# Performance work log

Measured on AMD Instinct MI355X. Metric: run time of the kernel, lower is better.

The kernel has to match this reference:

```python
import jax, jax.numpy as jnp
import numpy as np

# Module hyperparameters (from __init__ defaults / init_kwargs)
A_PLUS = 0.005
A_MINUS = 0.00525
TAU_PLUS = 20.0
TAU_MINUS = 20.0
DT = 1.0

B, T, N_PRE, N_POST = 512, 100, 256, 256
SPIKE_RATE = 0.1


def setup_inputs() -> dict:
    key = jax.random.key(0)
    k1, k2, k3 = jax.random.split(key, 3)
    pre_spikes = (jax.random.uniform(k1, (B, T, N_PRE)) < SPIKE_RATE).astype(jnp.float32)
    post_spikes = (jax.random.uniform(k2, (B, T, N_POST)) < SPIKE_RATE).astype(jnp.float32)
    weights = jax.random.uniform(k3, (N_PRE, N_POST), dtype=jnp.float32)
    return {"pre_spikes": pre_spikes, "post_spikes": post_spikes, "weights": weights}


def _pre_trace(pre_tbn, decay):
    """trace[t] = sum_{tau=1..t} decay^tau * pre[t-tau]  (exact recurrence).

    pre_tbn: [T, B, N]. Returns [T, B, N] with trace[0] = 0.
    """
    def step(carry, x_t):
        # emit trace[t] = carry, then carry' = decay * (carry + pre[t])
        return decay * (carry + x_t), carry
    _, trace = jax.lax.scan(step, jnp.zeros_like(pre_tbn[0]), pre_tbn)
    return trace


def reference(pre_spikes, post_spikes, weights):
    """Classical STDP weight update.

    With T <= int(tau_plus*5) the original nested t/tau loops equal:
      dW[p,q] = (1/(B*T)) * sum_{t,b} (A+ * trace+[t,b,p] - A- * trace-[t,b,p]) * post[b,t,q]
    where trace+/- are exponential pre-synaptic eligibility traces.
    """
    batch, time_steps, _ = pre_spikes.shape
    pre_t = jnp.transpose(pre_spikes, (1, 0, 2))    # [T, B, n_pre]
    post_t = jnp.transpose(post_spikes, (1, 0, 2))  # [T, B, n_post]

    decay_plus = jnp.exp(jnp.float32(-DT / TAU_PLUS))
    decay_minus = jnp.exp(jnp.float32(-DT / TAU_MINUS))

    trace_plus = _pre_trace(pre_t, decay_plus)    # LTP: pre fires before post
    trace_minus = _pre_trace(pre_t, decay_minus)  # LTD: pre fires before post (depression of reversed pairing)

    eff = A_PLUS * trace_plus - A_MINUS * trace_minus  # [T, B, n_pre]
    weight_update = jnp.einsum('tbp,tbq->pq', eff, post_t) / (batch * time_steps)
    # original initializes update as zeros_like(weights); output shape matches weights
    return weight_update + jnp.zeros_like(weights)
```

## Files before the change

kernel.cpp:

```cpp
#include <hip/hip_runtime.h>
#include <stdint.h>

#define B_SZ   512
#define T_SZ   100
#define NPRE   256
#define NPOST  256
#define KTOT   (B_SZ * T_SZ)

typedef __bf16 bf16x8 __attribute__((ext_vector_type(8)));
typedef float  floatx4 __attribute__((ext_vector_type(4)));

__device__ __forceinline__ uint32_t bf16_rne(float v) {
    uint32_t bits = __float_as_uint(v);
    return (bits + 0x7FFFu + ((bits >> 16) & 1u)) >> 16;
}
__device__ __forceinline__ uint32_t pack_trunc2(float a, float b) {
    return (__float_as_uint(a) >> 16) | (__float_as_uint(b) & 0xFFFF0000u);
}

__global__ __launch_bounds__(256, 2) void stdp_fused_gemm(
    const float* __restrict__ pre, const float* __restrict__ post,
    float* __restrict__ partial)
{
    __shared__ __align__(16) unsigned short A_lds[32][512];
    __shared__ __align__(16) unsigned short B_lds[32][512];

    const int bx   = blockIdx.x;
    const int s    = bx & 127;
    const int tile = bx >> 7;
    const int pt   = tile & 1;
    const int qt   = tile >> 1;
    const int tid  = threadIdx.x;
    const int lane = tid & 63, wave = tid >> 6;
    const int l15 = lane & 15, l4 = lane >> 4;

    const int half  = tid >> 7;
    const int p_loc = tid & 127;
    const int qloc  = tid & 127;
    const int qg = qloc >> 4, q15 = qloc & 15;

    const float decay = 0.95122942450071400910f;

    floatx4 acc[2][8] = {};

    for (int r = 0; r < 2; ++r) {
        uint32_t pk[50];
        {
            const int b = s * 4 + 2 * r + half;
            const float* src = pre + (size_t)b * (T_SZ * NPRE) + pt * 128 + p_loc;
            float carry = 0.0f;
#pragma unroll
            for (int kc = 0; kc < 3; ++kc) {
                float x[32];
#pragma unroll
                for (int j = 0; j < 32; ++j)
                    x[j] = src[(size_t)(kc * 32 + j) * NPRE];
#pragma unroll
                for (int j = 0; j < 16; ++j) {
                    uint32_t lo = bf16_rne(carry);
                    carry = decay * (carry + x[2 * j]);
                    uint32_t hi = bf16_rne(carry);
                    carry = decay * (carry + x[2 * j + 1]);
                    pk[kc * 16 + j] = lo | (hi << 16);
                }
            }
            float x[4];
#pragma unroll
            for (int j = 0; j < 4; ++j)
                x[j] = src[(size_t)(96 + j) * NPRE];
#pragma unroll
            for (int j = 0; j < 2; ++j) {
                uint32_t lo = bf16_rne(carry);
                carry = decay * (carry + x[2 * j]);
                uint32_t hi = bf16_rne(carry);
                carry = decay * (carry + x[2 * j + 1]);
                pk[48 + j] = lo | (hi << 16);
            }
        }

        for (int lh = 0; lh < 2; ++lh) {
            const int b = s * 4 + 2 * r + lh;

            if (half == lh) {
                const int pg = p_loc >> 4, lp = p_loc & 15;
#pragma unroll
                for (int kc = 0; kc < 3; ++kc)
#pragma unroll
                    for (int w = 0; w < 4; ++w)
                        *(uint4*)&A_lds[kc * 8 + pg][(w * 16 + lp) * 8] =
                            make_uint4(pk[kc * 16 + w * 4],     pk[kc * 16 + w * 4 + 1],
                                       pk[kc * 16 + w * 4 + 2], pk[kc * 16 + w * 4 + 3]);
                *(uint4*)&A_lds[24 + pg][lp * 8] = make_uint4(pk[48], pk[49], 0u, 0u);
#pragma unroll
                for (int w = 1; w < 4; ++w)
                    *(uint4*)&A_lds[24 + pg][(w * 16 + lp) * 8] =
                        make_uint4(0u, 0u, 0u, 0u);
            }

            const float* pb = post + (size_t)b * (T_SZ * NPOST) + qt * 128 + qloc;
            if (half == 0) {
                float x[48];
#pragma unroll
                for (int j = 0; j < 48; ++j)
                    x[j] = pb[(size_t)j * NPOST];
#pragma unroll
                for (int o = 0; o < 6; ++o)
                    *(uint4*)&B_lds[(o >> 2) * 8 + qg][((o & 3) * 16 + q15) * 8] =
                        make_uint4(pack_trunc2(x[o * 8 + 0], x[o * 8 + 1]),
                                   pack_trunc2(x[o * 8 + 2], x[o * 8 + 3]),
                                   pack_trunc2(x[o * 8 + 4], x[o * 8 + 5]),
                                   pack_trunc2(x[o * 8 + 6], x[o * 8 + 7]));
            } else {
                float x[52];
#pragma unroll
                for (int j = 0; j < 52; ++j)
                    x[j] = pb[(size_t)(48 + j) * NPOST];
#pragma unroll
                for (int o = 6; o < 12; ++o) {
                    int u = o * 8 - 48;
                    *(uint4*)&B_lds[(o >> 2) * 8 + qg][((o & 3) * 16 + q15) * 8] =
                        make_uint4(pack_trunc2(x[u + 0], x[u + 1]),
                                   pack_trunc2(x[u + 2], x[u + 3]),
                                   pack_trunc2(x[u + 4], x[u + 5]),
                                   pack_trunc2(x[u + 6], x[u + 7]));
                }
                *(uint4*)&B_lds[24 + qg][q15 * 8] =
                    make_uint4(pack_trunc2(x[48], x[49]), pack_trunc2(x[50], x[51]), 0u, 0u);
#pragma unroll
                for (int o = 13; o < 16; ++o)
                    *(uint4*)&B_lds[24 + qg][((o & 3) * 16 + q15) * 8] =
                        make_uint4(0u, 0u, 0u, 0u);
            }
            __syncthreads();

#pragma unroll
            for (int kc = 0; kc < 4; ++kc) {
                bf16x8 a[2], bb[8];
#pragma unroll
                for (int f = 0; f < 2; ++f)
                    a[f] = *(const bf16x8*)&A_lds[kc * 8 + wave * 2 + f][lane * 8];
#pragma unroll
                for (int g = 0; g < 8; ++g)
                    bb[g] = *(const bf16x8*)&B_lds[kc * 8 + g][lane * 8];
#pragma unroll
                for (int f = 0; f < 2; ++f)
#pragma unroll
                    for (int g = 0; g < 8; ++g)
                        acc[f][g] = __builtin_amdgcn_mfma_f32_16x16x32_bf16(
                            a[f], bb[g], acc[f][g], 0, 0, 0);
            }
            __syncthreads();
        }
    }

    float* pout = partial + (size_t)bx * (128 * 128);
#pragma unroll
    for (int f = 0; f < 2; ++f) {
        int r0 = wave * 32 + f * 16 + l4 * 4;
#pragma unroll
        for (int g = 0; g < 8; ++g) {
            int c = g * 16 + l15;
#pragma unroll
            for (int v = 0; v < 4; ++v)
                pout[(size_t)(r0 + v) * 128 + c] = acc[f][g][v];
        }
    }
}

__global__ __launch_bounds__(256) void stdp_reduce1(
    const float* __restrict__ partial, float* __restrict__ tmp)
{
    const int t = blockIdx.x * 256 + threadIdx.x;
    const int g = t >> 16;
    const int e = t & 65535;
    const int tile = e >> 14;
    const float* src = partial + ((size_t)(tile * 128 + g * 16) << 14) + (e & 16383);
    float a4[4] = {};
#pragma unroll
    for (int i = 0; i < 4; ++i)
#pragma unroll
        for (int u = 0; u < 4; ++u)
            a4[u] += src[(size_t)(u * 4 + i) << 14];
    tmp[t] = (a4[0] + a4[1]) + (a4[2] + a4[3]);
}

__global__ __launch_bounds__(256) void stdp_reduce2(
    const float* __restrict__ tmp, float* __restrict__ out)
{
    const int idx = blockIdx.x * 256 + threadIdx.x;
    const int P = idx >> 8, Q = idx & 255;
    const int tile = (Q >> 7) * 2 + (P >> 7);
    const int e = (tile << 14) | ((P & 127) << 7) | (Q & 127);
    float a[4];
#pragma unroll
    for (int u = 0; u < 4; ++u)
        a[u] = tmp[(size_t)(2 * u) * 65536 + e] +
               tmp[(size_t)(2 * u + 1) * 65536 + e];
    const float scale = (0.005f - 0.00525f) * (1.0f / (float)KTOT);
    out[idx] = ((a[0] + a[1]) + (a[2] + a[3])) * scale;
}

extern "C" void kernel_launch(void* const* d_in, const int* in_sizes, int n_in,
                              void* d_out, int out_size, void* d_ws, size_t ws_size,
                              hipStream_t stream)
{
    const float* pre  = (const float*)d_in[0];
    const float* post = (const float*)d_in[1];
    float* out = (float*)d_out;

    float* partial = (float*)d_ws;
    float* tmp     = (float*)((char*)d_ws + (size_t)33554432);

    stdp_fused_gemm<<<512, 256, 0, stream>>>(pre, post, partial);
    stdp_reduce1<<<2048, 256, 0, stream>>>(partial, tmp);
    stdp_reduce2<<<256, 256, 0, stream>>>(tmp, out);
}
```

Measured before the change: 140.4 us.

## Double block size to 512 threads, computing all four batch traces in one pass

The GEMM kernel now runs 512 threads per block. Each 128-thread group computes the pre-synaptic trace for one of the four batch elements in a single pass, instead of looping twice over pairs. Post-spike loading is split across four groups, and each wave now owns one 16-row slice with 8 accumulators instead of 2x8. The aim is more parallelism and fewer serial trace passes and register-heavy loads per thread, which should cut latency. The cost is larger blocks and the same number of barriers per batch element.

New measurement: 145.8 us. 1.04x slower.

```diff
diff --git a/kernel.cpp b/kernel.cpp
--- a/kernel.cpp
+++ b/kernel.cpp
@@ -18,7 +18,7 @@
     return (__float_as_uint(a) >> 16) | (__float_as_uint(b) & 0xFFFF0000u);
 }
 
-__global__ __launch_bounds__(256, 2) void stdp_fused_gemm(
+__global__ __launch_bounds__(512, 4) void stdp_fused_gemm(
     const float* __restrict__ pre, const float* __restrict__ post,
     float* __restrict__ partial)
 {
@@ -34,136 +34,124 @@
     const int lane = tid & 63, wave = tid >> 6;
     const int l15 = lane & 15, l4 = lane >> 4;
 
-    const int half  = tid >> 7;
+    const int grp   = tid >> 7;
     const int p_loc = tid & 127;
     const int qloc  = tid & 127;
     const int qg = qloc >> 4, q15 = qloc & 15;
+    const int pg = p_loc >> 4, lp = p_loc & 15;
 
     const float decay = 0.95122942450071400910f;
 
-    floatx4 acc[2][8] = {};
-
-    for (int r = 0; r < 2; ++r) {
-        uint32_t pk[50];
-        {
-            const int b = s * 4 + 2 * r + half;
-            const float* src = pre + (size_t)b * (T_SZ * NPRE) + pt * 128 + p_loc;
-            float carry = 0.0f;
-#pragma unroll
-            for (int kc = 0; kc < 3; ++kc) {
-                float x[32];
-#pragma unroll
-                for (int j = 0; j < 32; ++j)
-                    x[j] = src[(size_t)(kc * 32 + j) * NPRE];
-#pragma unroll
-                for (int j = 0; j < 16; ++j) {
-                    uint32_t lo = bf16_rne(carry);
-                    carry = decay * (carry + x[2 * j]);
-                    uint32_t hi = bf16_rne(carry);
-                    carry = decay * (carry + x[2 * j + 1]);
-                    pk[kc * 16 + j] = lo | (hi << 16);
-                }
-            }
-            float x[4];
-#pragma unroll
-            for (int j = 0; j < 4; ++j)
-                x[j] = src[(size_t)(96 + j) * NPRE];
-#pragma unroll
-            for (int j = 0; j < 2; ++j) {
+    uint32_t pk[50];
+    {
+        const int b = s * 4 + grp;
+        const float* src = pre + (size_t)b * (T_SZ * NPRE) + pt * 128 + p_loc;
+        float carry = 0.0f;
+#pragma unroll
+        for (int kc = 0; kc < 3; ++kc) {
+            float x[32];
+#pragma unroll
+            for (int j = 0; j < 32; ++j)
+                x[j] = src[(size_t)(kc * 32 + j) * NPRE];
+#pragma unroll
+            for (int j = 0; j < 16; ++j) {
                 uint32_t lo = bf16_rne(carry);
                 carry = decay * (carry + x[2 * j]);
                 uint32_t hi = bf16_rne(carry);
                 carry = decay * (carry + x[2 * j + 1]);
-                pk[48 + j] = lo | (hi << 16);
+                pk[kc * 16 + j] = lo | (hi << 16);
             }
         }
-
-        for (int lh = 0; lh < 2; ++lh) {
-            const int b = s * 4 + 2 * r + lh;
-
-            if (half == lh) {
-                const int pg = p_loc >> 4, lp = p_loc & 15;
-#pragma unroll
-                for (int kc = 0; kc < 3; ++kc)
-#pragma unroll
-                    for (int w = 0; w < 4; ++w)
-                        *(uint4*)&A_lds[kc * 8 + pg][(w * 16 + lp) * 8] =
-                            make_uint4(pk[kc * 16 + w * 4],     pk[kc * 16 + w * 4 + 1],
-                                       pk[kc * 16 + w * 4 + 2], pk[kc * 16 + w * 4 + 3]);
-                *(uint4*)&A_lds[24 + pg][lp * 8] = make_uint4(pk[48], pk[49], 0u, 0u);
-#pragma unroll
-                for (int w = 1; w < 4; ++w)
-                    *(uint4*)&A_lds[24 + pg][(w * 16 + lp) * 8] =
-                        make_uint4(0u, 0u, 0u, 0u);
+        float x[4];
+#pragma unroll
+        for (int j = 0; j < 4; ++j)
+            x[j] = src[(size_t)(96 + j) * NPRE];
+#pragma unroll
+        for (int j = 0; j < 2; ++j) {
+            uint32_t lo = bf16_rne(carry);
+            carry = decay * (carry + x[2 * j]);
+            uint32_t hi = bf16_rne(carry);
+            carry = decay * (carry + x[2 * j + 1]);
+            pk[48 + j] = lo | (hi << 16);
+        }
+    }
+
+    floatx4 acc[8] = {};
+
+#pragma unroll
+    for (int g = 0; g < 4; ++g) {
+        const int b = s * 4 + g;
+        if (g) __syncthreads();
+
+        if (grp == g) {
+#pragma unroll
+            for (int kc = 0; kc < 3; ++kc)
+#pragma unroll
+                for (int w = 0; w < 4; ++w)
+                    *(uint4*)&A_lds[kc * 8 + pg][(w * 16 + lp) * 8] =
+                        make_uint4(pk[kc * 16 + w * 4],     pk[kc * 16 + w * 4 + 1],
+                                   pk[kc * 16 + w * 4 + 2], pk[kc * 16 + w * 4 + 3]);
+            *(uint4*)&A_lds[24 + pg][lp * 8] = make_uint4(pk[48], pk[49], 0u, 0u);
+#pragma unroll
+            for (int w = 1; w < 4; ++w)
+                *(uint4*)&A_lds[24 + pg][(w * 16 + lp) * 8] =
+                    make_uint4(0u, 0u, 0u, 0u);
+        }
+
+        const float* pb = post + (size_t)b * (T_SZ * NPOST) + qt * 128 + qloc;
+        if (grp < 3) {
+#pragma unroll
+            for (int h = 0; h < 2; ++h) {
+                float x[16];
+#pragma unroll
+                for (int j = 0; j < 16; ++j)
+                    x[j] = pb[(size_t)(grp * 32 + h * 16 + j) * NPOST];
+#pragma unroll
+                for (int w2 = 0; w2 < 2; ++w2) {
+                    const int w = h * 2 + w2;
+                    *(uint4*)&B_lds[grp * 8 + qg][(w * 16 + q15) * 8] =
+                        make_uint4(pack_trunc2(x[w2 * 8 + 0], x[w2 * 8 + 1]),
+                                   pack_trunc2(x[w2 * 8 + 2], x[w2 * 8 + 3]),
+                                   pack_trunc2(x[w2 * 8 + 4], x[w2 * 8 + 5]),
+                                   pack_trunc2(x[w2 * 8 + 6], x[w2 * 8 + 7]));
+                }
             }
-
-            const float* pb = post + (size_t)b * (T_SZ * NPOST) + qt * 128 + qloc;
-            if (half == 0) {
-                float x[48];
-#pragma unroll
-                for (int j = 0; j < 48; ++j)
-                    x[j] = pb[(size_t)j * NPOST];
-#pragma unroll
-                for (int o = 0; o < 6; ++o)
-                    *(uint4*)&B_lds[(o >> 2) * 8 + qg][((o & 3) * 16 + q15) * 8] =
-                        make_uint4(pack_trunc2(x[o * 8 + 0], x[o * 8 + 1]),
-                                   pack_trunc2(x[o * 8 + 2], x[o * 8 + 3]),
-                                   pack_trunc2(x[o * 8 + 4], x[o * 8 + 5]),
-                                   pack_trunc2(x[o * 8 + 6], x[o * 8 + 7]));
-            } else {
-                float x[52];
-#pragma unroll
-                for (int j = 0; j < 52; ++j)
-                    x[j] = pb[(size_t)(48 + j) * NPOST];
-#pragma unroll
-                for (int o = 6; o < 12; ++o) {
-                    int u = o * 8 - 48;
-                    *(uint4*)&B_lds[(o >> 2) * 8 + qg][((o & 3) * 16 + q15) * 8] =
-                        make_uint4(pack_trunc2(x[u + 0], x[u + 1]),
-                                   pack_trunc2(x[u + 2], x[u + 3]),
-                                   pack_trunc2(x[u + 4], x[u + 5]),
-                                   pack_trunc2(x[u + 6], x[u + 7]));
-                }
-                *(uint4*)&B_lds[24 + qg][q15 * 8] =
-                    make_uint4(pack_trunc2(x[48], x[49]), pack_trunc2(x[50], x[51]), 0u, 0u);
-#pragma unroll
-                for (int o = 13; o < 16; ++o)
-                    *(uint4*)&B_lds[24 + qg][((o & 3) * 16 + q15) * 8] =
-                        make_uint4(0u, 0u, 0u, 0u);
-            }
-            __syncthreads();
-
-#pragma unroll
-            for (int kc = 0; kc < 4; ++kc) {
-                bf16x8 a[2], bb[8];
-#pragma unroll
-                for (int f = 0; f < 2; ++f)
-                    a[f] = *(const bf16x8*)&A_lds[kc * 8 + wave * 2 + f][lane * 8];
-#pragma unroll
-                for (int g = 0; g < 8; ++g)
-                    bb[g] = *(const bf16x8*)&B_lds[kc * 8 + g][lane * 8];
-#pragma unroll
-                for (int f = 0; f < 2; ++f)
-#pragma unroll
-                    for (int g = 0; g < 8; ++g)
-                        acc[f][g] = __builtin_amdgcn_mfma_f32_16x16x32_bf16(
-                            a[f], bb[g], acc[f][g], 0, 0, 0);
-            }
-            __syncthreads();
+        } else {
+            float x[4];
+#pragma unroll
+            for (int j = 0; j < 4; ++j)
+                x[j] = pb[(size_t)(96 + j) * NPOST];
+            *(uint4*)&B_lds[24 + qg][q15 * 8] =
+                make_uint4(pack_trunc2(x[0], x[1]), pack_trunc2(x[2], x[3]), 0u, 0u);
+#pragma unroll
+            for (int w = 1; w < 4; ++w)
+                *(uint4*)&B_lds[24 + qg][(w * 16 + q15) * 8] =
+                    make_uint4(0u, 0u, 0u, 0u);
+        }
+        __syncthreads();
+
+#pragma unroll
+        for (int kc = 0; kc < 4; ++kc) {
+            bf16x8 a = *(const bf16x8*)&A_lds[kc * 8 + wave][lane * 8];
+            bf16x8 bb[8];
+#pragma unroll
+            for (int gg = 0; gg < 8; ++gg)
+                bb[gg] = *(const bf16x8*)&B_lds[kc * 8 + gg][lane * 8];
+#pragma unroll
+            for (int gg = 0; gg < 8; ++gg)
+                acc[gg] = __builtin_amdgcn_mfma_f32_16x16x32_bf16(
+                    a, bb[gg], acc[gg], 0, 0, 0);
         }
     }
 
     float* pout = partial + (size_t)bx * (128 * 128);
-#pragma unroll
-    for (int f = 0; f < 2; ++f) {
-        int r0 = wave * 32 + f * 16 + l4 * 4;
-#pragma unroll
-        for (int g = 0; g < 8; ++g) {
-            int c = g * 16 + l15;
-#pragma unroll
-            for (int v = 0; v < 4; ++v)
-                pout[(size_t)(r0 + v) * 128 + c] = acc[f][g][v];
-        }
+    const int r0 = wave * 16 + l4 * 4;
+#pragma unroll
+    for (int gg = 0; gg < 8; ++gg) {
+        const int c = gg * 16 + l15;
+#pragma unroll
+        for (int v = 0; v < 4; ++v)
+            pout[(size_t)(r0 + v) * 128 + c] = acc[gg][v];
     }
 }
 
@@ -211,7 +199,7 @@
     float* partial = (float*)d_ws;
     float* tmp     = (float*)((char*)d_ws + (size_t)33554432);
 
-    stdp_fused_gemm<<<512, 256, 0, stream>>>(pre, post, partial);
+    stdp_fused_gemm<<<512, 512, 0, stream>>>(pre, post, partial);
     stdp_reduce1<<<2048, 256, 0, stream>>>(partial, tmp);
     stdp_reduce2<<<256, 256, 0, stream>>>(tmp, out);
 }
```

## Software-pipeline global loads of pre/post spikes across scan and MFMA phases

Applied to the files above, without the earlier changes.

Restructures the fused scan+GEMM kernel so global loads for the next time chunks, the next batch's post spikes and the next round's pre spikes are issued before the current data is consumed. Scheduling barriers pin the load placement so the loads overlap the trace scan and the MFMA loop. The launch-bounds occupancy hint is replaced with an amdgpu_waves_per_eu attribute. This raises register pressure (several prefetch buffers held live) and may cause spills or reduced occupancy.

Result: slower. 190.1 us (+35.4%).

```diff
diff --git a/kernel.cpp b/kernel.cpp
--- a/kernel.cpp
+++ b/kernel.cpp
@@ -18,7 +18,83 @@
     return (__float_as_uint(a) >> 16) | (__float_as_uint(b) & 0xFFFF0000u);
 }
 
-__global__ __launch_bounds__(256, 2) void stdp_fused_gemm(
+__device__ __forceinline__ void issue_x(const float* src, int tbase, int n, float* x) {
+#pragma unroll
+    for (int j = 0; j < n; ++j)
+        x[j] = src[(size_t)(tbase + j) * NPRE];
+}
+
+__device__ __forceinline__ void consume16(const float* x, float& carry,
+                                          uint32_t* pkc, float decay) {
+#pragma unroll
+    for (int j = 0; j < 16; ++j) {
+        uint32_t lo = bf16_rne(carry);
+        carry = decay * (carry + x[2 * j]);
+        uint32_t hi = bf16_rne(carry);
+        carry = decay * (carry + x[2 * j + 1]);
+        pkc[j] = lo | (hi << 16);
+    }
+}
+
+__device__ __forceinline__ void deposit_A(unsigned short (*A)[512],
+                                          const uint32_t* pk, int pg, int lp)
+{
+#pragma unroll
+    for (int kc = 0; kc < 3; ++kc)
+#pragma unroll
+        for (int w = 0; w < 4; ++w)
+            *(uint4*)&A[kc * 8 + pg][(w * 16 + lp) * 8] =
+                make_uint4(pk[kc * 16 + w * 4],     pk[kc * 16 + w * 4 + 1],
+                           pk[kc * 16 + w * 4 + 2], pk[kc * 16 + w * 4 + 3]);
+    *(uint4*)&A[24 + pg][lp * 8] = make_uint4(pk[48], pk[49], 0u, 0u);
+#pragma unroll
+    for (int w = 1; w < 4; ++w)
+        *(uint4*)&A[24 + pg][(w * 16 + lp) * 8] = make_uint4(0u, 0u, 0u, 0u);
+}
+
+__device__ __forceinline__ void load_B(const float* pb, int half, float* x) {
+    if (half == 0) {
+#pragma unroll
+        for (int j = 0; j < 48; ++j)
+            x[j] = pb[(size_t)j * NPOST];
+    } else {
+#pragma unroll
+        for (int j = 0; j < 52; ++j)
+            x[j] = pb[(size_t)(48 + j) * NPOST];
+    }
+}
+__device__ __forceinline__ void store_B(unsigned short (*Bl)[512], int half,
+                                        int qg, int q15, const float* x)
+{
+    if (half == 0) {
+#pragma unroll
+        for (int o = 0; o < 6; ++o)
+            *(uint4*)&Bl[(o >> 2) * 8 + qg][((o & 3) * 16 + q15) * 8] =
+                make_uint4(pack_trunc2(x[o * 8 + 0], x[o * 8 + 1]),
+                           pack_trunc2(x[o * 8 + 2], x[o * 8 + 3]),
+                           pack_trunc2(x[o * 8 + 4], x[o * 8 + 5]),
+                           pack_trunc2(x[o * 8 + 6], x[o * 8 + 7]));
+    } else {
+#pragma unroll
+        for (int o = 6; o < 12; ++o) {
+            int u = o * 8 - 48;
+            *(uint4*)&Bl[(o >> 2) * 8 + qg][((o & 3) * 16 + q15) * 8] =
+                make_uint4(pack_trunc2(x[u + 0], x[u + 1]),
+                           pack_trunc2(x[u + 2], x[u + 3]),
+                           pack_trunc2(x[u + 4], x[u + 5]),
+                           pack_trunc2(x[u + 6], x[u + 7]));
+        }
+        *(uint4*)&Bl[24 + qg][q15 * 8] =
+            make_uint4(pack_trunc2(x[48], x[49]), pack_trunc2(x[50], x[51]), 0u, 0u);
+#pragma unroll
+        for (int o = 13; o < 16; ++o)
+            *(uint4*)&Bl[24 + qg][((o & 3) * 16 + q15) * 8] =
+                make_uint4(0u, 0u, 0u, 0u);
+    }
+}
+
+__global__ __launch_bounds__(256) __attribute__((amdgpu_waves_per_eu(2)))
+void stdp_fused_gemm(
     const float* __restrict__ pre, const float* __restrict__ post,
     float* __restrict__ partial)
 {
@@ -38,119 +114,103 @@
     const int p_loc = tid & 127;
     const int qloc  = tid & 127;
     const int qg = qloc >> 4, q15 = qloc & 15;
+    const int pg = p_loc >> 4, lp = p_loc & 15;
 
     const float decay = 0.95122942450071400910f;
 
     floatx4 acc[2][8] = {};
 
+    float x0[32], x1[32], x2[36], xb[52];
+    uint32_t pk[50];
+
+    {
+        const int b = s * 4 + half;
+        const float* src = pre + (size_t)b * (T_SZ * NPRE) + pt * 128 + p_loc;
+        issue_x(src, 0, 32, x0);
+        __builtin_amdgcn_sched_barrier(0);
+        issue_x(src, 32, 32, x1);
+        __builtin_amdgcn_sched_barrier(0);
+    }
+
+#pragma unroll
     for (int r = 0; r < 2; ++r) {
-        uint32_t pk[50];
-        {
-            const int b = s * 4 + 2 * r + half;
-            const float* src = pre + (size_t)b * (T_SZ * NPRE) + pt * 128 + p_loc;
-            float carry = 0.0f;
-#pragma unroll
-            for (int kc = 0; kc < 3; ++kc) {
-                float x[32];
-#pragma unroll
-                for (int j = 0; j < 32; ++j)
-                    x[j] = src[(size_t)(kc * 32 + j) * NPRE];
-#pragma unroll
-                for (int j = 0; j < 16; ++j) {
-                    uint32_t lo = bf16_rne(carry);
-                    carry = decay * (carry + x[2 * j]);
-                    uint32_t hi = bf16_rne(carry);
-                    carry = decay * (carry + x[2 * j + 1]);
-                    pk[kc * 16 + j] = lo | (hi << 16);
-                }
-            }
-            float x[4];
-#pragma unroll
-            for (int j = 0; j < 4; ++j)
-                x[j] = src[(size_t)(96 + j) * NPRE];
-#pragma unroll
-            for (int j = 0; j < 2; ++j) {
-                uint32_t lo = bf16_rne(carry);
-                carry = decay * (carry + x[2 * j]);
-                uint32_t hi = bf16_rne(carry);
-                carry = decay * (carry + x[2 * j + 1]);
-                pk[48 + j] = lo | (hi << 16);
-            }
-        }
-
-        for (int lh = 0; lh < 2; ++lh) {
-            const int b = s * 4 + 2 * r + lh;
-
-            if (half == lh) {
-                const int pg = p_loc >> 4, lp = p_loc & 15;
-#pragma unroll
-                for (int kc = 0; kc < 3; ++kc)
-#pragma unroll
-                    for (int w = 0; w < 4; ++w)
-                        *(uint4*)&A_lds[kc * 8 + pg][(w * 16 + lp) * 8] =
-                            make_uint4(pk[kc * 16 + w * 4],     pk[kc * 16 + w * 4 + 1],
-                                       pk[kc * 16 + w * 4 + 2], pk[kc * 16 + w * 4 + 3]);
-                *(uint4*)&A_lds[24 + pg][lp * 8] = make_uint4(pk[48], pk[49], 0u, 0u);
-#pragma unroll
-                for (int w = 1; w < 4; ++w)
-                    *(uint4*)&A_lds[24 + pg][(w * 16 + lp) * 8] =
-                        make_uint4(0u, 0u, 0u, 0u);
-            }
-
-            const float* pb = post + (size_t)b * (T_SZ * NPOST) + qt * 128 + qloc;
-            if (half == 0) {
-                float x[48];
-#pragma unroll
-                for (int j = 0; j < 48; ++j)
-                    x[j] = pb[(size_t)j * NPOST];
-#pragma unroll
-                for (int o = 0; o < 6; ++o)
-                    *(uint4*)&B_lds[(o >> 2) * 8 + qg][((o & 3) * 16 + q15) * 8] =
-                        make_uint4(pack_trunc2(x[o * 8 + 0], x[o * 8 + 1]),
-                                   pack_trunc2(x[o * 8 + 2], x[o * 8 + 3]),
-                                   pack_trunc2(x[o * 8 + 4], x[o * 8 + 5]),
-                                   pack_trunc2(x[o * 8 + 6], x[o * 8 + 7]));
-            } else {
-                float x[52];
-#pragma unroll
-                for (int j = 0; j < 52; ++j)
-                    x[j] = pb[(size_t)(48 + j) * NPOST];
-#pragma unroll
-                for (int o = 6; o < 12; ++o) {
-                    int u = o * 8 - 48;
-                    *(uint4*)&B_lds[(o >> 2) * 8 + qg][((o & 3) * 16 + q15) * 8] =
-                        make_uint4(pack_trunc2(x[u + 0], x[u + 1]),
-                                   pack_trunc2(x[u + 2], x[u + 3]),
-                                   pack_trunc2(x[u + 4], x[u + 5]),
-                                   pack_trunc2(x[u + 6], x[u + 7]));
-                }
-                *(uint4*)&B_lds[24 + qg][q15 * 8] =
-                    make_uint4(pack_trunc2(x[48], x[49]), pack_trunc2(x[50], x[51]), 0u, 0u);
-#pragma unroll
-                for (int o = 13; o < 16; ++o)
-                    *(uint4*)&B_lds[24 + qg][((o & 3) * 16 + q15) * 8] =
-                        make_uint4(0u, 0u, 0u, 0u);
-            }
-            __syncthreads();
-
-#pragma unroll
-            for (int kc = 0; kc < 4; ++kc) {
-                bf16x8 a[2], bb[8];
-#pragma unroll
-                for (int f = 0; f < 2; ++f)
-                    a[f] = *(const bf16x8*)&A_lds[kc * 8 + wave * 2 + f][lane * 8];
+        const int b_scan = s * 4 + 2 * r + half;
+        const float* src = pre + (size_t)b_scan * (T_SZ * NPRE) + pt * 128 + p_loc;
+        float carry = 0.0f;
+
+        consume16(x0, carry, &pk[0], decay);
+        issue_x(src, 64, 36, x2);
+        __builtin_amdgcn_sched_barrier(0);
+        consume16(x1, carry, &pk[16], decay);
+        load_B(post + (size_t)(s * 4 + 2 * r) * (T_SZ * NPOST) + qt * 128 + qloc,
+               half, xb);
+        __builtin_amdgcn_sched_barrier(0);
+        consume16(x2, carry, &pk[32], decay);
+#pragma unroll
+        for (int j = 0; j < 2; ++j) {
+            uint32_t lo = bf16_rne(carry);
+            carry = decay * (carry + x2[32 + 2 * j]);
+            uint32_t hi = bf16_rne(carry);
+            carry = decay * (carry + x2[32 + 2 * j + 1]);
+            pk[48 + j] = lo | (hi << 16);
+        }
+
+        if (half == 0) deposit_A(A_lds, pk, pg, lp);
+        store_B(B_lds, half, qg, q15, xb);
+        __syncthreads();
+
+        load_B(post + (size_t)(s * 4 + 2 * r + 1) * (T_SZ * NPOST) + qt * 128 + qloc,
+               half, xb);
+        __builtin_amdgcn_sched_barrier(0);
+
+#pragma unroll
+        for (int kc = 0; kc < 4; ++kc) {
+            bf16x8 a[2], bb[8];
+#pragma unroll
+            for (int f = 0; f < 2; ++f)
+                a[f] = *(const bf16x8*)&A_lds[kc * 8 + wave * 2 + f][lane * 8];
+#pragma unroll
+            for (int g = 0; g < 8; ++g)
+                bb[g] = *(const bf16x8*)&B_lds[kc * 8 + g][lane * 8];
+#pragma unroll
+            for (int f = 0; f < 2; ++f)
 #pragma unroll
                 for (int g = 0; g < 8; ++g)
-                    bb[g] = *(const bf16x8*)&B_lds[kc * 8 + g][lane * 8];
-#pragma unroll
-                for (int f = 0; f < 2; ++f)
-#pragma unroll
-                    for (int g = 0; g < 8; ++g)
-                        acc[f][g] = __builtin_amdgcn_mfma_f32_16x16x32_bf16(
-                            a[f], bb[g], acc[f][g], 0, 0, 0);
-            }
-            __syncthreads();
-        }
+                    acc[f][g] = __builtin_amdgcn_mfma_f32_16x16x32_bf16(
+                        a[f], bb[g], acc[f][g], 0, 0, 0);
+        }
+        __syncthreads();
+
+        if (half == 1) deposit_A(A_lds, pk, pg, lp);
+        store_B(B_lds, half, qg, q15, xb);
+        __syncthreads();
+
+        if (r == 0) {
+            const int bn = s * 4 + 2 + half;
+            const float* srcn = pre + (size_t)bn * (T_SZ * NPRE) + pt * 128 + p_loc;
+            issue_x(srcn, 0, 32, x0);
+            __builtin_amdgcn_sched_barrier(0);
+            issue_x(srcn, 32, 32, x1);
+            __builtin_amdgcn_sched_barrier(0);
+        }
+
+#pragma unroll
+        for (int kc = 0; kc < 4; ++kc) {
+            bf16x8 a[2], bb[8];
+#pragma unroll
+            for (int f = 0; f < 2; ++f)
+                a[f] = *(const bf16x8*)&A_lds[kc * 8 + wave * 2 + f][lane * 8];
+#pragma unroll
+            for (int g = 0; g < 8; ++g)
+                bb[g] = *(const bf16x8*)&B_lds[kc * 8 + g][lane * 8];
+#pragma unroll
+            for (int f = 0; f < 2; ++f)
+#pragma unroll
+                for (int g = 0; g < 8; ++g)
+                    acc[f][g] = __builtin_amdgcn_mfma_f32_16x16x32_bf16(
+                        a[f], bb[g], acc[f][g], 0, 0, 0);
+        }
+        __syncthreads();
     }
 
     float* pout = partial + (size_t)bx * (128 * 128);
```

## Split batch work across twice as many blocks with halved LDS staging

Applied to the files above, without the earlier changes.

The GEMM grid grows from 512 to 1024 blocks, so each block handles 2 batch elements instead of 4. Time is split into two K halves, which halves the LDS tiles, and a waves-per-EU hint targets higher occupancy. Within a phase one half of the threads builds the pre-trace A tile while the other half converts the post B tile, where before both halves did the post work. This aims to hide global-load latency through more parallelism, at the cost of twice as many partial tiles written to and read back by the reduction kernel.

Result: slower. 157.3 us (+12.0%).

```diff
diff --git a/kernel.cpp b/kernel.cpp
--- a/kernel.cpp
+++ b/kernel.cpp
@@ -18,139 +18,143 @@
     return (__float_as_uint(a) >> 16) | (__float_as_uint(b) & 0xFFFF0000u);
 }
 
-__global__ __launch_bounds__(256, 2) void stdp_fused_gemm(
+__global__ __launch_bounds__(256) __attribute__((amdgpu_waves_per_eu(4, 4)))
+void stdp_fused_gemm(
     const float* __restrict__ pre, const float* __restrict__ post,
     float* __restrict__ partial)
 {
-    __shared__ __align__(16) unsigned short A_lds[32][512];
-    __shared__ __align__(16) unsigned short B_lds[32][512];
+    __shared__ __align__(16) unsigned short A_lds[16][512];
+    __shared__ __align__(16) unsigned short B_lds[16][512];
 
     const int bx   = blockIdx.x;
-    const int s    = bx & 127;
-    const int tile = bx >> 7;
+    const int s2   = bx & 255;
+    const int tile = bx >> 8;
     const int pt   = tile & 1;
     const int qt   = tile >> 1;
     const int tid  = threadIdx.x;
     const int lane = tid & 63, wave = tid >> 6;
     const int l15 = lane & 15, l4 = lane >> 4;
 
-    const int half  = tid >> 7;
-    const int p_loc = tid & 127;
-    const int qloc  = tid & 127;
-    const int qg = qloc >> 4, q15 = qloc & 15;
+    const int bh   = tid >> 7;
+    const int nloc = tid & 127;
+    const int ng = nloc >> 4, n15 = nloc & 15;
 
     const float decay = 0.95122942450071400910f;
 
+    float carry = 0.0f;
     floatx4 acc[2][8] = {};
 
-    for (int r = 0; r < 2; ++r) {
-        uint32_t pk[50];
-        {
-            const int b = s * 4 + 2 * r + half;
-            const float* src = pre + (size_t)b * (T_SZ * NPRE) + pt * 128 + p_loc;
-            float carry = 0.0f;
-#pragma unroll
-            for (int kc = 0; kc < 3; ++kc) {
-                float x[32];
-#pragma unroll
-                for (int j = 0; j < 32; ++j)
-                    x[j] = src[(size_t)(kc * 32 + j) * NPRE];
-#pragma unroll
-                for (int j = 0; j < 16; ++j) {
-                    uint32_t lo = bf16_rne(carry);
-                    carry = decay * (carry + x[2 * j]);
-                    uint32_t hi = bf16_rne(carry);
-                    carry = decay * (carry + x[2 * j + 1]);
-                    pk[kc * 16 + j] = lo | (hi << 16);
+#pragma unroll
+    for (int ph = 0; ph < 4; ++ph) {
+        const int b = ph >> 1, h = ph & 1;
+        const int bglob = 2 * s2 + b;
+
+        if (bh == b) {
+            if (h == 0) carry = 0.0f;
+            const float* src = pre + (size_t)bglob * (T_SZ * NPRE)
+                                   + pt * 128 + nloc;
+#pragma unroll
+            for (int kc2 = 0; kc2 < 2; ++kc2) {
+                if (h == 0 || kc2 == 0) {
+                    float x[32];
+#pragma unroll
+                    for (int j = 0; j < 32; ++j)
+                        x[j] = src[(size_t)(h * 64 + kc2 * 32 + j) * NPRE];
+#pragma unroll
+                    for (int w = 0; w < 4; ++w) {
+                        uint32_t u[4];
+#pragma unroll
+                        for (int m = 0; m < 4; ++m) {
+                            uint32_t lo = bf16_rne(carry);
+                            carry = decay * (carry + x[w * 8 + 2 * m]);
+                            uint32_t hi = bf16_rne(carry);
+                            carry = decay * (carry + x[w * 8 + 2 * m + 1]);
+                            u[m] = lo | (hi << 16);
+                        }
+                        *(uint4*)&A_lds[kc2 * 8 + ng][(w * 16 + n15) * 8] =
+                            make_uint4(u[0], u[1], u[2], u[3]);
+                    }
+                } else {
+                    float x[4];
+#pragma unroll
+                    for (int j = 0; j < 4; ++j)
+                        x[j] = src[(size_t)(96 + j) * NPRE];
+                    uint32_t u0, u1;
+                    {
+                        uint32_t lo = bf16_rne(carry);
+                        carry = decay * (carry + x[0]);
+                        uint32_t hi = bf16_rne(carry);
+                        carry = decay * (carry + x[1]);
+                        u0 = lo | (hi << 16);
+                    }
+                    {
+                        uint32_t lo = bf16_rne(carry);
+                        carry = decay * (carry + x[2]);
+                        uint32_t hi = bf16_rne(carry);
+                        carry = decay * (carry + x[3]);
+                        u1 = lo | (hi << 16);
+                    }
+                    *(uint4*)&A_lds[8 + ng][n15 * 8] = make_uint4(u0, u1, 0u, 0u);
+#pragma unroll
+                    for (int w = 1; w < 4; ++w)
+                        *(uint4*)&A_lds[8 + ng][(w * 16 + n15) * 8] =
+                            make_uint4(0u, 0u, 0u, 0u);
                 }
             }
-            float x[4];
-#pragma unroll
-            for (int j = 0; j < 4; ++j)
-                x[j] = src[(size_t)(96 + j) * NPRE];
-#pragma unroll
-            for (int j = 0; j < 2; ++j) {
-                uint32_t lo = bf16_rne(carry);
-                carry = decay * (carry + x[2 * j]);
-                uint32_t hi = bf16_rne(carry);
-                carry = decay * (carry + x[2 * j + 1]);
-                pk[48 + j] = lo | (hi << 16);
+        } else {
+            const float* pb = post + (size_t)bglob * (T_SZ * NPOST)
+                                   + qt * 128 + nloc;
+#pragma unroll
+            for (int kc2 = 0; kc2 < 2; ++kc2) {
+                if (h == 0 || kc2 == 0) {
+                    float y[32];
+#pragma unroll
+                    for (int j = 0; j < 32; ++j)
+                        y[j] = pb[(size_t)(h * 64 + kc2 * 32 + j) * NPOST];
+#pragma unroll
+                    for (int w = 0; w < 4; ++w) {
+                        uint32_t u[4];
+#pragma unroll
+                        for (int m = 0; m < 4; ++m)
+                            u[m] = pack_trunc2(y[w * 8 + 2 * m],
+                                               y[w * 8 + 2 * m + 1]);
+                        *(uint4*)&B_lds[kc2 * 8 + ng][(w * 16 + n15) * 8] =
+                            make_uint4(u[0], u[1], u[2], u[3]);
+                    }
+                } else {
+                    float y[4];
+#pragma unroll
+                    for (int j = 0; j < 4; ++j)
+                        y[j] = pb[(size_t)(96 + j) * NPOST];
+                    *(uint4*)&B_lds[8 + ng][n15 * 8] =
+                        make_uint4(pack_trunc2(y[0], y[1]),
+                                   pack_trunc2(y[2], y[3]), 0u, 0u);
+#pragma unroll
+                    for (int w = 1; w < 4; ++w)
+                        *(uint4*)&B_lds[8 + ng][(w * 16 + n15) * 8] =
+                            make_uint4(0u, 0u, 0u, 0u);
+                }
             }
         }
-
-        for (int lh = 0; lh < 2; ++lh) {
-            const int b = s * 4 + 2 * r + lh;
-
-            if (half == lh) {
-                const int pg = p_loc >> 4, lp = p_loc & 15;
-#pragma unroll
-                for (int kc = 0; kc < 3; ++kc)
-#pragma unroll
-                    for (int w = 0; w < 4; ++w)
-                        *(uint4*)&A_lds[kc * 8 + pg][(w * 16 + lp) * 8] =
-                            make_uint4(pk[kc * 16 + w * 4],     pk[kc * 16 + w * 4 + 1],
-                                       pk[kc * 16 + w * 4 + 2], pk[kc * 16 + w * 4 + 3]);
-                *(uint4*)&A_lds[24 + pg][lp * 8] = make_uint4(pk[48], pk[49], 0u, 0u);
-#pragma unroll
-                for (int w = 1; w < 4; ++w)
-                    *(uint4*)&A_lds[24 + pg][(w * 16 + lp) * 8] =
-                        make_uint4(0u, 0u, 0u, 0u);
-            }
-
-            const float* pb = post + (size_t)b * (T_SZ * NPOST) + qt * 128 + qloc;
-            if (half == 0) {
-                float x[48];
-#pragma unroll
-                for (int j = 0; j < 48; ++j)
-                    x[j] = pb[(size_t)j * NPOST];
-#pragma unroll
-                for (int o = 0; o < 6; ++o)
-                    *(uint4*)&B_lds[(o >> 2) * 8 + qg][((o & 3) * 16 + q15) * 8] =
-                        make_uint4(pack_trunc2(x[o * 8 + 0], x[o * 8 + 1]),
-                                   pack_trunc2(x[o * 8 + 2], x[o * 8 + 3]),
-                                   pack_trunc2(x[o * 8 + 4], x[o * 8 + 5]),
-                                   pack_trunc2(x[o * 8 + 6], x[o * 8 + 7]));
-            } else {
-                float x[52];
-#pragma unroll
-                for (int j = 0; j < 52; ++j)
-                    x[j] = pb[(size_t)(48 + j) * NPOST];
-#pragma unroll
-                for (int o = 6; o < 12; ++o) {
-                    int u = o * 8 - 48;
-                    *(uint4*)&B_lds[(o >> 2) * 8 + qg][((o & 3) * 16 + q15) * 8] =
-                        make_uint4(pack_trunc2(x[u + 0], x[u + 1]),
-                                   pack_trunc2(x[u + 2], x[u + 3]),
-                                   pack_trunc2(x[u + 4], x[u + 5]),
-                                   pack_trunc2(x[u + 6], x[u + 7]));
-                }
-                *(uint4*)&B_lds[24 + qg][q15 * 8] =
-                    make_uint4(pack_trunc2(x[48], x[49]), pack_trunc2(x[50], x[51]), 0u, 0u);
-#pragma unroll
-                for (int o = 13; o < 16; ++o)
-                    *(uint4*)&B_lds[24 + qg][((o & 3) * 16 + q15) * 8] =
-                        make_uint4(0u, 0u, 0u, 0u);
-            }
-            __syncthreads();
-
-#pragma unroll
-            for (int kc = 0; kc < 4; ++kc) {
-                bf16x8 a[2], bb[8];
-#pragma unroll
-                for (int f = 0; f < 2; ++f)
-                    a[f] = *(const bf16x8*)&A_lds[kc * 8 + wave * 2 + f][lane * 8];
+        __syncthreads();
+
+#pragma unroll
+        for (int kc = 0; kc < 2; ++kc) {
+            bf16x8 a[2], bb[8];
+#pragma unroll
+            for (int f = 0; f < 2; ++f)
+                a[f] = *(const bf16x8*)&A_lds[kc * 8 + wave * 2 + f][lane * 8];
+#pragma unroll
+            for (int g = 0; g < 8; ++g)
+                bb[g] = *(const bf16x8*)&B_lds[kc * 8 + g][lane * 8];
+#pragma unroll
+            for (int f = 0; f < 2; ++f)
 #pragma unroll
                 for (int g = 0; g < 8; ++g)
-                    bb[g] = *(const bf16x8*)&B_lds[kc * 8 + g][lane * 8];
-#pragma unroll
-                for (int f = 0; f < 2; ++f)
-#pragma unroll
-                    for (int g = 0; g < 8; ++g)
-                        acc[f][g] = __builtin_amdgcn_mfma_f32_16x16x32_bf16(
-                            a[f], bb[g], acc[f][g], 0, 0, 0);
-            }
-            __syncthreads();
+                    acc[f][g] = __builtin_amdgcn_mfma_f32_16x16x32_bf16(
+                        a[f], bb[g], acc[f][g], 0, 0, 0);
         }
+        __syncthreads();
     }
 
     float* pout = partial + (size_t)bx * (128 * 128);
@@ -174,13 +178,13 @@
     const int g = t >> 16;
     const int e = t & 65535;
     const int tile = e >> 14;
-    const float* src = partial + ((size_t)(tile * 128 + g * 16) << 14) + (e & 16383);
+    const float* src = partial + ((size_t)(tile * 256 + g * 32) << 14) + (e & 16383);
     float a4[4] = {};
 #pragma unroll
-    for (int i = 0; i < 4; ++i)
+    for (int i = 0; i < 8; ++i)
 #pragma unroll
         for (int u = 0; u < 4; ++u)
-            a4[u] += src[(size_t)(u * 4 + i) << 14];
+            a4[u] += src[(size_t)(u * 8 + i) << 14];
     tmp[t] = (a4[0] + a4[1]) + (a4[2] + a4[3]);
 }
 
@@ -209,9 +213,9 @@
     float* out = (float*)d_out;
 
     float* partial = (float*)d_ws;
-    float* tmp     = (float*)((char*)d_ws + (size_t)33554432);
-
-    stdp_fused_gemm<<<512, 256, 0, stream>>>(pre, post, partial);
+    float* tmp     = (float*)((char*)d_ws + (size_t)67108864);
+
+    stdp_fused_gemm<<<1024, 256, 0, stream>>>(pre, post, partial);
     stdp_reduce1<<<2048, 256, 0, stream>>>(partial, tmp);
     stdp_reduce2<<<256, 256, 0, stream>>>(tmp, out);
 }
```
